# Kernel optimization log

Hardware: AMD Instinct MI355X
Metric: run time of the kernel (lower is better)

The kernel has to match this reference:

```python
import jax, jax.numpy as jnp
import numpy as np

N_NODES = 100000
N_EDGES = 3200000
N_GRAPHS = 4096
IN_DIM = 128
HID = 64
EPS = 1e-5


def setup_inputs() -> dict:
    key = jax.random.key(0)
    ks = jax.random.split(key, 16)
    x = jax.random.normal(ks[0], (N_NODES, IN_DIM), dtype=jnp.float32)
    edge_index = jax.random.randint(ks[1], (2, N_EDGES), 0, N_NODES, dtype=jnp.int32)
    batch = jnp.sort(jax.random.randint(ks[2], (N_NODES,), 0, N_GRAPHS, dtype=jnp.int32))

    def lin(k, fan_in, fan_out):
        s = 1.0 / np.sqrt(fan_in)
        kw, kb = jax.random.split(k)
        W = jax.random.uniform(kw, (fan_in, fan_out), minval=-s, maxval=s, dtype=jnp.float32)
        b = jax.random.uniform(kb, (fan_out,), minval=-s, maxval=s, dtype=jnp.float32)
        return W, b

    Wc0, bc0 = lin(ks[3], IN_DIM, HID)
    Wc1, bc1 = lin(ks[4], HID, HID)
    Wc2, bc2 = lin(ks[5], HID, HID)
    W1, b1 = lin(ks[6], HID, HID)
    W2, b2 = lin(ks[7], HID, 1)
    ones = jnp.ones((HID,), jnp.float32)
    zeros = jnp.zeros((HID,), jnp.float32)
    return {
        'x': x, 'edge_index': edge_index, 'batch': batch,
        'Wc0': Wc0, 'bc0': bc0, 'g0': ones, 'be0': zeros,
        'Wc1': Wc1, 'bc1': bc1, 'g1': ones, 'be1': zeros,
        'Wc2': Wc2, 'bc2': bc2, 'g2': ones, 'be2': zeros,
        'W1': W1, 'b1': b1, 'gf': ones, 'bf': zeros,
        'W2': W2, 'b2': b2,
    }


def _gcn_norm(edge_index):
    # Add self-loops, then symmetric normalization norm_e = d^-1/2[row] * d^-1/2[col]
    loops = jnp.arange(N_NODES, dtype=jnp.int32)
    row = jnp.concatenate([edge_index[0], loops])
    col = jnp.concatenate([edge_index[1], loops])
    deg = jax.ops.segment_sum(jnp.ones_like(col, jnp.float32), col, num_segments=N_NODES)
    dinv = jnp.where(deg > 0, jax.lax.rsqrt(deg), 0.0)
    norm = dinv[row] * dinv[col]
    return row, col, norm


def _gcn_conv(x, W, b, row, col, norm):
    h = x @ W                                   # [N, hid]
    msg = h[row] * norm[:, None]                # [E+N, hid] gather + scale
    out = jax.ops.segment_sum(msg, col, num_segments=N_NODES)  # scatter-add
    return out + b


def _bn(x, gamma, beta):
    mu = jnp.mean(x, axis=0)
    var = jnp.var(x, axis=0)
    return (x - mu) * jax.lax.rsqrt(var + EPS) * gamma + beta


def reference(x, edge_index, batch, Wc0, bc0, g0, be0, Wc1, bc1, g1, be1,
              Wc2, bc2, g2, be2, W1, b1, gf, bf, W2, b2):
    row, col, norm = _gcn_norm(edge_index)
    h = x
    for W, b, g, be in ((Wc0, bc0, g0, be0), (Wc1, bc1, g1, be1), (Wc2, bc2, g2, be2)):
        h = jax.nn.relu(_bn(_gcn_conv(h, W, b, row, col, norm), g, be))
    # global mean pool over graphs
    sums = jax.ops.segment_sum(h, batch, num_segments=N_GRAPHS)
    cnts = jax.ops.segment_sum(jnp.ones((N_NODES,), jnp.float32), batch, num_segments=N_GRAPHS)
    pooled = sums / jnp.maximum(cnts, 1.0)[:, None]  # [G, hid]
    z = jax.nn.relu(_bn(pooled @ W1 + b1, gf, bf))
    # dropout is identity at inference
    out = z @ W2 + b2
    return out.squeeze(-1)
```

## Files before the change

### kernel.cpp

```cpp
#include <hip/hip_runtime.h>
#include <hip/hip_bf16.h>

#define NN 100000
#define NE 3200000
#define NG 4096
#define NB 256
#define NBK 782

typedef unsigned short ushort_t;
typedef short short8 __attribute__((ext_vector_type(8)));
typedef float floatx4 __attribute__((ext_vector_type(4)));

__device__ __forceinline__ float bf2f(unsigned short u){
  union{unsigned int i; float f;} x; x.i = ((unsigned)u)<<16; return x.f;
}
__device__ __forceinline__ ushort_t f2bf(float f){
  union{float f; unsigned int i;} x; x.f = f;
  unsigned int r = x.i + 0x7fff + ((x.i >> 16) & 1);
  return (ushort_t)(r >> 16);
}


__global__ __launch_bounds__(512) void k_hist(const int* __restrict__ ei, int* __restrict__ histT){
  __shared__ int lh[NBK];
  int b = blockIdx.x, t = threadIdx.x;
  for (int k=t; k<NBK; k+=512) lh[k]=0;
  __syncthreads();
  int e0 = b*(NE/NB);
  for (int e=e0+t; e<e0+(NE/NB); e+=512) atomicAdd(&lh[ei[NE+e]>>7], 1);
  __syncthreads();
  for (int k=t; k<NBK; k+=512) histT[(size_t)k*NB+b] = lh[k];
}

__global__ __launch_bounds__(256) void k_scanA(int* __restrict__ histT, int* __restrict__ total){
  int wv = blockIdx.x*4 + (threadIdx.x>>6);
  int lane = threadIdx.x & 63;
  if (wv >= NBK) return;
  int* row = histT + (size_t)wv*NB;
  int carry = 0;
  #pragma unroll
  for (int ch=0; ch<NB/64; ++ch){
    int a = row[ch*64+lane];
    int inc = a;
    for (int off=1; off<64; off<<=1){
      int x = __shfl_up(inc, off, 64);
      if (lane >= off) inc += x;
    }
    row[ch*64+lane] = carry + inc - a;
    carry += __shfl(inc, 63, 64);
  }
  if (lane==0) total[wv] = carry;
}

__global__ void k_scanB(const int* __restrict__ total, int* __restrict__ base){
  __shared__ int lds[1024];
  int t = threadIdx.x;
  int v = (t < NBK)? total[t] : 0;
  lds[t] = v; __syncthreads();
  for (int off=1; off<1024; off<<=1){
    int x = (t>=off)? lds[t-off] : 0;
    __syncthreads();
    lds[t] += x;
    __syncthreads();
  }
  if (t < NBK)      base[t]   = lds[t]-v;
  if (t == NBK-1)   base[NBK] = lds[t];
}

__global__ __launch_bounds__(512) void k_pairs(const int* __restrict__ ei,
    const int* __restrict__ histT, const int* __restrict__ base,
    int* __restrict__ pairs){
  __shared__ int cur[NBK];
  int b = blockIdx.x, t = threadIdx.x;
  for (int k=t; k<NBK; k+=512) cur[k] = base[k] + histT[(size_t)k*NB + b];
  __syncthreads();
  int e0 = b*(NE/NB);
  for (int e=e0+t; e<e0+(NE/NB); e+=512){
    int src = ei[e], dst = ei[NE+e];
    int p = atomicAdd(&cur[dst>>7], 1);
    pairs[p] = (src << 7) | (dst & 127);
  }
}

__global__ __launch_bounds__(256) void k_fine(const int* __restrict__ pairs,
    const int* __restrict__ base, int* __restrict__ csr,
    int* __restrict__ colptr, float* __restrict__ dinv){
  __shared__ int cnt[128], off[128];
  int k = blockIdx.x, t = threadIdx.x;
  if (t < 128) cnt[t] = 0;
  __syncthreads();
  int s = base[k], e = base[k+1];
  for (int i=s+t; i<e; i+=256) atomicAdd(&cnt[pairs[i] & 127], 1);
  __syncthreads();
  int v = (t<128)? cnt[t] : 0;
  if (t<128) off[t] = v;
  __syncthreads();
  for (int o=1; o<128; o<<=1){
    int x = (t>=o && t<128)? off[t-o] : 0;
    __syncthreads();
    if (t<128) off[t] += x;
    __syncthreads();
  }
  int node0 = k*128;
  if (t < 128 && node0+t < NN){
    colptr[node0+t] = s + off[t] - v;
    dinv[node0+t]   = rsqrtf((float)cnt[t] + 1.0f);
  }
  if (k == NBK-1 && t == 0) colptr[NN] = NE;
  __syncthreads();
  if (t < 128) cnt[t] = off[t] - v;
  __syncthreads();
  for (int i=s+t; i<e; i+=256){
    int u = pairs[i];
    int p = s + atomicAdd(&cnt[u & 127], 1);
    csr[p] = u >> 7;
  }
}


__global__ __launch_bounds__(256) void k_gemm0m(const float* __restrict__ x,
    const float* __restrict__ W, const float* __restrict__ dinv,
    ushort_t* __restrict__ hs){
  __shared__ __attribute__((aligned(16))) ushort_t Wt[64*136];
  int t = threadIdx.x;
  for (int i=t; i<128*64; i+=256){
    int k = i>>6, n = i&63;
    Wt[n*136 + k] = f2bf(W[i]);
  }
  __syncthreads();
  int lane = t & 63, wv = t >> 6;
  int n0 = lane & 15, quad = lane >> 4;
  int r0 = blockIdx.x*64 + wv*16;
  int row = r0 + n0;
  int rowc = (row < NN)? row : NN-1;
  const float* xr = x + (size_t)rowc*128 + quad*8;
  floatx4 acc[4] = {{0,0,0,0},{0,0,0,0},{0,0,0,0},{0,0,0,0}};
  #pragma unroll
  for (int ks=0; ks<4; ++ks){
    float4 a01 = *(const float4*)(xr + ks*32);
    float4 a23 = *(const float4*)(xr + ks*32 + 4);
    short8 af;
    af[0]=(short)f2bf(a01.x); af[1]=(short)f2bf(a01.y);
    af[2]=(short)f2bf(a01.z); af[3]=(short)f2bf(a01.w);
    af[4]=(short)f2bf(a23.x); af[5]=(short)f2bf(a23.y);
    af[6]=(short)f2bf(a23.z); af[7]=(short)f2bf(a23.w);
    #pragma unroll
    for (int tl=0; tl<4; ++tl){
      short8 bf = *(const short8*)(&Wt[(tl*16+n0)*136 + ks*32 + quad*8]);
      acc[tl] = __builtin_amdgcn_mfma_f32_16x16x32_bf16(af, bf, acc[tl], 0, 0, 0);
    }
  }
  #pragma unroll
  for (int reg=0; reg<4; ++reg){
    int rr = r0 + quad*4 + reg;
    if (rr < NN){
      float dv = dinv[rr];
      #pragma unroll
      for (int tl=0; tl<4; ++tl)
        hs[(size_t)rr*64 + tl*16 + n0] = f2bf(acc[tl][reg]*dv);
    }
  }
}


__global__ __launch_bounds__(256) void k_gemmSm(const float* __restrict__ h,
    const float* __restrict__ W, const float* __restrict__ coeff,
    const float* __restrict__ dinv, ushort_t* __restrict__ hs){
  __shared__ __attribute__((aligned(16))) ushort_t Wt[64*72];
  int t = threadIdx.x;
  for (int i=t; i<64*64; i+=256){
    int k = i>>6, n = i&63;
    Wt[n*72 + k] = f2bf(W[i]);
  }
  __syncthreads();
  int lane = t & 63, wv = t >> 6;
  int n0 = lane & 15, quad = lane >> 4;
  int r0 = blockIdx.x*64 + wv*16;
  int row = r0 + n0;
  int rowc = (row < NN)? row : NN-1;
  const float* hr = h + (size_t)rowc*64 + quad*8;
  floatx4 acc[4] = {{0,0,0,0},{0,0,0,0},{0,0,0,0},{0,0,0,0}};
  #pragma unroll
  for (int ks=0; ks<2; ++ks){
    float4 a01 = *(const float4*)(hr + ks*32);
    float4 a23 = *(const float4*)(hr + ks*32 + 4);
    const float* cA = coeff + ks*32 + quad*8;
    float4 ca0 = *(const float4*)(cA),      ca1 = *(const float4*)(cA+4);
    float4 cb0 = *(const float4*)(cA+64),   cb1 = *(const float4*)(cA+68);
    short8 af;
    af[0]=(short)f2bf(fmaxf(fmaf(a01.x,ca0.x,cb0.x),0.f));
    af[1]=(short)f2bf(fmaxf(fmaf(a01.y,ca0.y,cb0.y),0.f));
    af[2]=(short)f2bf(fmaxf(fmaf(a01.z,ca0.z,cb0.z),0.f));
    af[3]=(short)f2bf(fmaxf(fmaf(a01.w,ca0.w,cb0.w),0.f));
    af[4]=(short)f2bf(fmaxf(fmaf(a23.x,ca1.x,cb1.x),0.f));
    af[5]=(short)f2bf(fmaxf(fmaf(a23.y,ca1.y,cb1.y),0.f));
    af[6]=(short)f2bf(fmaxf(fmaf(a23.z,ca1.z,cb1.z),0.f));
    af[7]=(short)f2bf(fmaxf(fmaf(a23.w,ca1.w,cb1.w),0.f));
    #pragma unroll
    for (int tl=0; tl<4; ++tl){
      short8 bf = *(const short8*)(&Wt[(tl*16+n0)*72 + ks*32 + quad*8]);
      acc[tl] = __builtin_amdgcn_mfma_f32_16x16x32_bf16(af, bf, acc[tl], 0, 0, 0);
    }
  }
  #pragma unroll
  for (int reg=0; reg<4; ++reg){
    int rr = r0 + quad*4 + reg;
    if (rr < NN){
      float dv = dinv[rr];
      #pragma unroll
      for (int tl=0; tl<4; ++tl)
        hs[(size_t)rr*64 + tl*16 + n0] = f2bf(acc[tl][reg]*dv);
    }
  }
}


__global__ __launch_bounds__(256) void k_aggregate(const ushort_t* __restrict__ hs,
    const int* __restrict__ colptr, const int* __restrict__ csr,
    const float* __restrict__ dinv, const float* __restrict__ bias,
    float* __restrict__ out, float* __restrict__ stats){
  int t = threadIdx.x; int c = t & 63;
  int wv = blockIdx.x*4 + (t>>6);
  float bc = bias[c];
  float s1 = 0.f, s2 = 0.f;
  for (int v = wv; v < NN; v += 8192){
    int vv = __builtin_amdgcn_readfirstlane(v);
    int e0 = colptr[vv], e1 = colptr[vv+1];
    float acc = bf2f(hs[(size_t)vv*64 + c]);
    int e = e0;
    for (; e+8 <= e1; e += 8){
      int i0=csr[e],   i1=csr[e+1], i2=csr[e+2], i3=csr[e+3];
      int i4=csr[e+4], i5=csr[e+5], i6=csr[e+6], i7=csr[e+7];
      float f0=bf2f(hs[(size_t)i0*64+c]), f1=bf2f(hs[(size_t)i1*64+c]);
      float f2=bf2f(hs[(size_t)i2*64+c]), f3=bf2f(hs[(size_t)i3*64+c]);
      float f4=bf2f(hs[(size_t)i4*64+c]), f5=bf2f(hs[(size_t)i5*64+c]);
      float f6=bf2f(hs[(size_t)i6*64+c]), f7=bf2f(hs[(size_t)i7*64+c]);
      acc += ((f0+f1)+(f2+f3)) + ((f4+f5)+(f6+f7));
    }
    for (; e+4 <= e1; e += 4){
      int i0=csr[e], i1=csr[e+1], i2=csr[e+2], i3=csr[e+3];
      float f0=bf2f(hs[(size_t)i0*64+c]), f1=bf2f(hs[(size_t)i1*64+c]);
      float f2=bf2f(hs[(size_t)i2*64+c]), f3=bf2f(hs[(size_t)i3*64+c]);
      acc += (f0+f1)+(f2+f3);
    }
    for (; e<e1; ++e) acc += bf2f(hs[(size_t)csr[e]*64+c]);
    float o = acc*dinv[vv] + bc;
    __builtin_nontemporal_store(o, &out[(size_t)vv*64+c]);
    s1 += o; s2 += o*o;
  }
  __shared__ float l1[256], l2[256];
  l1[t]=s1; l2[t]=s2; __syncthreads();
  if (t < 64){
    float a1 = l1[t]+l1[t+64]+l1[t+128]+l1[t+192];
    float a2 = l2[t]+l2[t+64]+l2[t+128]+l2[t+192];
    float* rep = stats + (size_t)(blockIdx.x & 31)*128;
    atomicAdd(&rep[t],    a1);
    atomicAdd(&rep[64+t], a2);
  }
}


__global__ void k_bncoeff(const float* __restrict__ stats, const float* __restrict__ g,
                          const float* __restrict__ be, float cnt, float* __restrict__ coeff){
  int c = threadIdx.x;
  float s1=0.f, s2=0.f;
  for (int r=0;r<32;++r){ s1 += stats[r*128+c]; s2 += stats[r*128+64+c]; }
  float mu  = s1/cnt;
  float var = s2/cnt - mu*mu;
  float a   = g[c]*rsqrtf(var + 1e-5f);
  coeff[c]    = a;
  coeff[64+c] = be[c] - mu*a;
}


__global__ __launch_bounds__(256) void k_poolhead(const float* __restrict__ h,
    const int* __restrict__ batch, const float* __restrict__ cf,
    const float* __restrict__ W1, const float* __restrict__ b1,
    float* __restrict__ tbuf, float* __restrict__ stats){
  __shared__ float pl[256];
  int t=threadIdx.x; int c=t&63; int wv=t>>6;
  int g = __builtin_amdgcn_readfirstlane((int)(blockIdx.x*4 + wv));
  int lo=0, hi=NN;
  while (lo<hi){ int mid=(lo+hi)>>1; if (batch[mid]<g) lo=mid+1; else hi=mid; }
  int s = lo;
  hi = NN;
  while (lo<hi){ int mid=(lo+hi)>>1; if (batch[mid]<g+1) lo=mid+1; else hi=mid; }
  int e = lo;
  float a = cf[c], d = cf[64+c];
  float acc=0.f;
  for (int v=s; v<e; ++v) acc += fmaxf(fmaf(h[(size_t)v*64+c], a, d), 0.f);
  float inv = 1.0f / fmaxf((float)(e-s), 1.0f);
  pl[wv*64 + c] = acc*inv;
  __syncthreads();
  const float* p = pl + wv*64;
  float tk = b1[c];
  #pragma unroll 4
  for (int k=0;k<64;++k) tk = fmaf(p[k], W1[k*64+c], tk);
  tbuf[(size_t)g*64+c] = tk;
  float* rep = stats + (size_t)(blockIdx.x & 31)*128;
  atomicAdd(&rep[c],    tk);
  atomicAdd(&rep[64+c], tk*tk);
}

__global__ __launch_bounds__(256) void k_final(const float* __restrict__ tbuf, const float* __restrict__ gcf,
                                               const float* __restrict__ W2, const float* __restrict__ b2,
                                               float* __restrict__ out){
  int t=threadIdx.x; int c=t&63;
  int g = blockIdx.x*4 + (t>>6);
  float tv = tbuf[(size_t)g*64+c];
  float z  = fmaxf(fmaf(tv, gcf[c], gcf[64+c]), 0.f);
  float p  = z * W2[c];
  #pragma unroll
  for (int o=32;o>0;o>>=1) p += __shfl_xor(p, o, 64);
  if (c==0) out[g] = p + b2[0];
}


extern "C" void kernel_launch(void* const* d_in, const int* in_sizes, int n_in,
                              void* d_out, int out_size, void* d_ws, size_t ws_size,
                              hipStream_t stream) {
  const float* x    = (const float*)d_in[0];
  const int*   ei   = (const int*)d_in[1];
  const int*   batch= (const int*)d_in[2];
  const float* Wc0=(const float*)d_in[3],  *bc0=(const float*)d_in[4];
  const float* g0 =(const float*)d_in[5],  *be0=(const float*)d_in[6];
  const float* Wc1=(const float*)d_in[7],  *bc1=(const float*)d_in[8];
  const float* g1 =(const float*)d_in[9],  *be1=(const float*)d_in[10];
  const float* Wc2=(const float*)d_in[11], *bc2=(const float*)d_in[12];
  const float* g2 =(const float*)d_in[13], *be2=(const float*)d_in[14];
  const float* W1 =(const float*)d_in[15], *b1 =(const float*)d_in[16];
  const float* gf =(const float*)d_in[17], *bf_=(const float*)d_in[18];
  const float* W2 =(const float*)d_in[19], *b2 =(const float*)d_in[20];
  float* out = (float*)d_out;

  char* w = (char*)d_ws;
  float*    stats  = (float*)   (w + 0);
  int*      total  = (int*)     (w + 65536);
  int*      base   = (int*)     (w + 68736);
  int*      colptr = (int*)     (w + 71936);
  float*    dinv   = (float*)   (w + 471952);
  float*    coeff  = (float*)   (w + 871952);
  float*    gcoeff = (float*)   (w + 872464);
  float*    pooled = (float*)   (w + 872976);
  int*      csr    = (int*)     (w + 1921552);
  ushort_t* bufA   = (ushort_t*)(w + 14721552);
  float*    bufB   = (float*)   (w + 27521552);
  int*      histT  = csr;
  int*      pairs  = (int*)bufB;

  hipMemsetAsync(stats, 0, 65536, stream);

  k_hist <<<NB,  512,  0, stream>>>(ei, histT);
  k_scanA<<<196, 256,  0, stream>>>(histT, total);
  k_scanB<<<1,   1024, 0, stream>>>(total, base);
  k_pairs<<<NB,  512,  0, stream>>>(ei, histT, base, pairs);
  k_fine <<<NBK, 256,  0, stream>>>(pairs, base, csr, colptr, dinv);

  k_gemm0m<<<1563, 256, 0, stream>>>(x, Wc0, dinv, bufA);
  k_aggregate<<<2048, 256, 0, stream>>>(bufA, colptr, csr, dinv, bc0, bufB, stats + 0*4096);
  k_bncoeff<<<1, 64, 0, stream>>>(stats + 0*4096, g0, be0, (float)NN, coeff);
  k_gemmSm<<<1563, 256, 0, stream>>>(bufB, Wc1, coeff, dinv, bufA);
  k_aggregate<<<2048, 256, 0, stream>>>(bufA, colptr, csr, dinv, bc1, bufB, stats + 1*4096);
  k_bncoeff<<<1, 64, 0, stream>>>(stats + 1*4096, g1, be1, (float)NN, coeff);
  k_gemmSm<<<1563, 256, 0, stream>>>(bufB, Wc2, coeff, dinv, bufA);
  k_aggregate<<<2048, 256, 0, stream>>>(bufA, colptr, csr, dinv, bc2, bufB, stats + 2*4096);
  k_bncoeff<<<1, 64, 0, stream>>>(stats + 2*4096, g2, be2, (float)NN, coeff);

  k_poolhead<<<NG/4, 256, 0, stream>>>(bufB, batch, coeff, W1, b1, pooled, stats + 3*4096);
  k_bncoeff<<<1, 64, 0, stream>>>(stats + 3*4096, gf, bf_, (float)NG, gcoeff);
  k_final<<<NG/4, 256, 0, stream>>>(pooled, gcoeff, W2, b2, out);
}
```

Baseline: 546.0 us.

## Sort CSR neighbors by source chunk and aggregate chunk-by-chunk for L2 locality

The CSR build now orders each node's neighbor list by source-index chunk (7 chunks of 16K nodes) through a finer 1024-bin counting sort. The aggregation kernel gives each wavefront 13 destination nodes spread over per-XCD contiguous node ranges. It walks all of them one source chunk at a time, so the concurrent gathers touch a bounded slice of hs that can stay resident in cache. The cost is more registers (13 accumulators and edge cursors), extra chunk-boundary branching, and a larger shared-memory scan in k_fine.

```diff
diff --git a/kernel.cpp b/kernel.cpp
--- a/kernel.cpp
+++ b/kernel.cpp
@@ -6,6 +6,8 @@
 #define NG 4096
 #define NB 256
 #define NBK 782
+#define NCHUNK 7
+#define CHSH 14
 
 typedef unsigned short ushort_t;
 typedef short short8 __attribute__((ext_vector_type(8)));
@@ -85,35 +87,46 @@
 __global__ __launch_bounds__(256) void k_fine(const int* __restrict__ pairs,
     const int* __restrict__ base, int* __restrict__ csr,
     int* __restrict__ colptr, float* __restrict__ dinv){
-  __shared__ int cnt[128], off[128];
+  __shared__ int cnt[1024], off[1024], part[256];
   int k = blockIdx.x, t = threadIdx.x;
-  if (t < 128) cnt[t] = 0;
+  for (int i=t; i<1024; i+=256) cnt[i]=0;
   __syncthreads();
   int s = base[k], e = base[k+1];
-  for (int i=s+t; i<e; i+=256) atomicAdd(&cnt[pairs[i] & 127], 1);
-  __syncthreads();
-  int v = (t<128)? cnt[t] : 0;
-  if (t<128) off[t] = v;
-  __syncthreads();
-  for (int o=1; o<128; o<<=1){
-    int x = (t>=o && t<128)? off[t-o] : 0;
+  for (int i=s+t; i<e; i+=256){
+    int u = pairs[i];
+    atomicAdd(&cnt[((u & 127) << 3) | ((u >> 7) >> CHSH)], 1);
+  }
+  __syncthreads();
+  int c0=cnt[t*4], c1=cnt[t*4+1], c2=cnt[t*4+2], c3=cnt[t*4+3];
+  int loc = c0+c1+c2+c3;
+  part[t] = loc;
+  __syncthreads();
+  for (int o=1; o<256; o<<=1){
+    int x = (t>=o)? part[t-o] : 0;
     __syncthreads();
-    if (t<128) off[t] += x;
+    part[t] += x;
     __syncthreads();
   }
+  int ex = part[t] - loc;
+  off[t*4]   = ex;
+  off[t*4+1] = ex + c0;
+  off[t*4+2] = ex + c0 + c1;
+  off[t*4+3] = ex + c0 + c1 + c2;
+  __syncthreads();
   int node0 = k*128;
   if (t < 128 && node0+t < NN){
-    colptr[node0+t] = s + off[t] - v;
-    dinv[node0+t]   = rsqrtf((float)cnt[t] + 1.0f);
+    int st = off[t*8];
+    int en = (t<127)? off[(t+1)*8] : (e-s);
+    colptr[node0+t] = s + st;
+    dinv[node0+t]   = rsqrtf((float)(en-st) + 1.0f);
   }
   if (k == NBK-1 && t == 0) colptr[NN] = NE;
-  __syncthreads();
-  if (t < 128) cnt[t] = off[t] - v;
   __syncthreads();
   for (int i=s+t; i<e; i+=256){
     int u = pairs[i];
-    int p = s + atomicAdd(&cnt[u & 127], 1);
-    csr[p] = u >> 7;
+    int src = u >> 7;
+    int p = s + atomicAdd(&off[((u & 127) << 3) | (src >> CHSH)], 1);
+    csr[p] = src;
   }
 }
 
@@ -220,33 +233,58 @@
     const float* __restrict__ dinv, const float* __restrict__ bias,
     float* __restrict__ out, float* __restrict__ stats){
   int t = threadIdx.x; int c = t & 63;
-  int wv = blockIdx.x*4 + (t>>6);
+  int b = blockIdx.x;
+  int xcd = b & 7;
+  int local = (b>>3)*4 + (t>>6);
+  int vb = xcd * (NN/8);
   float bc = bias[c];
+  float acc[13];
+  int E[13], Eend[13];
+  #pragma unroll
+  for (int j=0; j<13; ++j){
+    int idx = local + j*1024;
+    bool ok = idx < NN/8;
+    int v = __builtin_amdgcn_readfirstlane(vb + (ok? idx : 0));
+    float sv = bf2f(hs[(size_t)v*64 + c]);
+    acc[j] = ok? sv : 0.f;
+    int e0 = colptr[v];
+    E[j]    = e0;
+    Eend[j] = ok? colptr[v+1] : e0;
+  }
+  for (int ch=0; ch<NCHUNK; ++ch){
+    #pragma unroll
+    for (int j=0; j<13; ++j){
+      int e = E[j], e1 = Eend[j];
+      float a = 0.f;
+      while (e < e1){
+        if (e+4 <= e1){
+          int i0=csr[e], i1=csr[e+1], i2=csr[e+2], i3=csr[e+3];
+          if ((i3>>CHSH) == ch){
+            float f0=bf2f(hs[(size_t)i0*64+c]), f1=bf2f(hs[(size_t)i1*64+c]);
+            float f2=bf2f(hs[(size_t)i2*64+c]), f3=bf2f(hs[(size_t)i3*64+c]);
+            a += (f0+f1)+(f2+f3);
+            e += 4; continue;
+          }
+        }
+        int i0 = csr[e];
+        if ((i0>>CHSH) != ch) break;
+        a += bf2f(hs[(size_t)i0*64+c]);
+        ++e;
+      }
+      acc[j] += a;
+      E[j] = e;
+    }
+  }
   float s1 = 0.f, s2 = 0.f;
-  for (int v = wv; v < NN; v += 8192){
-    int vv = __builtin_amdgcn_readfirstlane(v);
-    int e0 = colptr[vv], e1 = colptr[vv+1];
-    float acc = bf2f(hs[(size_t)vv*64 + c]);
-    int e = e0;
-    for (; e+8 <= e1; e += 8){
-      int i0=csr[e],   i1=csr[e+1], i2=csr[e+2], i3=csr[e+3];
-      int i4=csr[e+4], i5=csr[e+5], i6=csr[e+6], i7=csr[e+7];
-      float f0=bf2f(hs[(size_t)i0*64+c]), f1=bf2f(hs[(size_t)i1*64+c]);
-      float f2=bf2f(hs[(size_t)i2*64+c]), f3=bf2f(hs[(size_t)i3*64+c]);
-      float f4=bf2f(hs[(size_t)i4*64+c]), f5=bf2f(hs[(size_t)i5*64+c]);
-      float f6=bf2f(hs[(size_t)i6*64+c]), f7=bf2f(hs[(size_t)i7*64+c]);
-      acc += ((f0+f1)+(f2+f3)) + ((f4+f5)+(f6+f7));
-    }
-    for (; e+4 <= e1; e += 4){
-      int i0=csr[e], i1=csr[e+1], i2=csr[e+2], i3=csr[e+3];
-      float f0=bf2f(hs[(size_t)i0*64+c]), f1=bf2f(hs[(size_t)i1*64+c]);
-      float f2=bf2f(hs[(size_t)i2*64+c]), f3=bf2f(hs[(size_t)i3*64+c]);
-      acc += (f0+f1)+(f2+f3);
-    }
-    for (; e<e1; ++e) acc += bf2f(hs[(size_t)csr[e]*64+c]);
-    float o = acc*dinv[vv] + bc;
-    __builtin_nontemporal_store(o, &out[(size_t)vv*64+c]);
-    s1 += o; s2 += o*o;
+  #pragma unroll
+  for (int j=0; j<13; ++j){
+    int idx = local + j*1024;
+    if (idx < NN/8){
+      int v = vb + idx;
+      float o = acc[j]*dinv[v] + bc;
+      __builtin_nontemporal_store(o, &out[(size_t)v*64+c]);
+      s1 += o; s2 += o*o;
+    }
   }
   __shared__ float l1[256], l2[256];
   l1[t]=s1; l2[t]=s2; __syncthreads();
```

Result: slower. 1.492 ms (+173.4%).
